# Performance work log

Hardware: AMD Instinct MI355X
Metric: run time of the kernel (lower is better)

## Reference

```python
import jax, jax.numpy as jnp
import numpy as np

B, S, VD, MD = 32, 2048, 512, 512
AD = max(VD, MD)


def setup_inputs() -> dict:
    key = jax.random.key(0)
    k1, k2, k3, k4, k5, k6 = jax.random.split(key, 6)
    query = jax.random.normal(k1, (B, VD), dtype=jnp.float32)
    keys = jax.random.normal(k2, (B, S, MD), dtype=jnp.float32)
    mask = jax.random.randint(k3, (B, S), 0, 2).astype(jnp.bool_)
    # torch Linear weight layout: [out, in]
    W1 = jax.random.normal(k4, (AD, VD), dtype=jnp.float32) * (1.0 / np.sqrt(VD))
    W2 = jax.random.normal(k5, (AD, MD), dtype=jnp.float32) * (1.0 / np.sqrt(MD))
    v = jax.random.normal(k6, (AD,), dtype=jnp.float32) * (1.0 / np.sqrt(AD))
    return {"query": query, "keys": keys, "mask": mask, "W1": W1, "W2": W2, "v": v}


def reference(query, keys, mask, W1, W2, v):
    # w1_query: [B, 1, AD]; w2_keys: [B, S, AD]
    w1_query = jnp.einsum('bd,ad->ba', query, W1)[:, None, :]
    w2_keys = jnp.einsum('bsd,ad->bsa', keys, W2)
    combined = jnp.tanh(w1_query + w2_keys)            # [B, S, AD]
    scores = jnp.einsum('bsa,a->bs', combined, v)      # [B, S]
    scores = jnp.where(mask, scores, -jnp.inf)
    attn_weights = jax.nn.softmax(scores, axis=-1)
    return attn_weights
```

## Files before the change

### kernel.cpp

```cpp
#include <hip/hip_runtime.h>
#include <math.h>

#define BB 32
#define SS 2048
#define DD 512
#define AD 512

#define BM 128
#define BN 128
#define BK 64

typedef __bf16 bf16;
typedef __attribute__((ext_vector_type(8))) __bf16 bf16x8;
typedef __attribute__((ext_vector_type(4))) __bf16 bf16x4;
typedef __attribute__((ext_vector_type(4))) float floatx4;

__device__ inline void async16(const void* g, void* l) {
    __builtin_amdgcn_global_load_lds(
        (const __attribute__((address_space(1))) unsigned int*)g,
        (__attribute__((address_space(3))) unsigned int*)l, 16, 0, 0);
}

#define NW8 (AD * DD / 8)
#define NCV (NW8 / 256)
__global__ void prep_kernel(const float* __restrict__ W2,
                            bf16* __restrict__ W2b,
                            const unsigned char* __restrict__ m8,
                            int* __restrict__ flag,
                            const float* __restrict__ query,
                            const float* __restrict__ W1,
                            float* __restrict__ w1q) {
    const int bid = blockIdx.x;
    if (bid < NCV) {
        int j = threadIdx.x + bid * 256;
        const float4* s4 = (const float4*)W2 + (size_t)j * 2;
        float4 x = s4[0], y = s4[1];
        bf16x8 o;
        o[0] = (bf16)x.x; o[1] = (bf16)x.y; o[2] = (bf16)x.z; o[3] = (bf16)x.w;
        o[4] = (bf16)y.x; o[5] = (bf16)y.y; o[6] = (bf16)y.z; o[7] = (bf16)y.w;
        *(bf16x8*)(W2b + (size_t)j * 8) = o;
    } else if (bid < NCV + 64) {
        int t = threadIdx.x + (bid - NCV) * 256;
        int any = 0;
        for (int i = t; i < BB * SS; i += 64 * 256)
            if ((i & 3) && m8[i]) any = 1;
        if (__any(any)) {
            if ((threadIdx.x & 63) == 0) atomicOr(flag, 1);
        }
    } else {
        int id = bid - NCV - 64;
        int b = id >> 7;
        int a = (id & 127) * 4 + (threadIdx.x >> 6);
        int lane = threadIdx.x & 63;
        const float4* q4 = (const float4*)(query + (size_t)b * DD) + lane * 2;
        const float4* w4 = (const float4*)(W1 + (size_t)a * DD) + lane * 2;
        float4 qa = q4[0], qb = q4[1];
        float4 wa = w4[0], wb = w4[1];
        float acc = qa.x * wa.x + qa.y * wa.y + qa.z * wa.z + qa.w * wa.w
                  + qb.x * wb.x + qb.y * wb.y + qb.z * wb.z + qb.w * wb.w;
#pragma unroll
        for (int off = 32; off > 0; off >>= 1) acc += __shfl_down(acc, off);
        if (lane == 0) w1q[(size_t)b * AD + a] = acc;
    }
}

__global__ __launch_bounds__(256, 3)
void gemm_scores_mfma(const float* __restrict__ keys,
                      const bf16* __restrict__ W2b,
                      const float* __restrict__ w1q,
                      const float* __restrict__ v,
                      float* __restrict__ partial) {
    __shared__ float a_lds[BM * BK];
    __shared__ bf16  b_lds[BN * BK];

    const int t    = threadIdx.x;
    const int lane = t & 63;
    const int w    = t >> 6;
    const int ml   = lane & 15;
    const int kg   = lane >> 4;

    const int lin    = blockIdx.x;
    const int x8     = lin & 7;
    const int hi     = lin >> 3;
    const int a_tile = hi & 3;
    const int kt     = x8 + ((hi >> 2) << 3);
    const int b      = kt >> 4;
    const int s0     = (kt & 15) * BM;
    const int a0     = a_tile * BN;

    const int m_off = (w & 1) * 64;
    const int n_off = (w >> 1) * 64;

    const float* Ablk = keys + ((size_t)b * SS + s0) * DD;
    const bf16*  Bblk = W2b + (size_t)a0 * DD;

    floatx4 acc[4][4];
#pragma unroll
    for (int mi = 0; mi < 4; ++mi)
#pragma unroll
        for (int ni = 0; ni < 4; ++ni)
            acc[mi][ni] = (floatx4)(0.f);

    const int NCHUNK = DD / BK;
    for (int c = 0; c < NCHUNK; ++c) {
        const int d0 = c * BK;
        __syncthreads();
#pragma unroll
        for (int i = 0; i < 8; ++i) {
            int g = t + 256 * i;
            int r = g >> 4, cc = g & 15, cs = cc ^ (r & 15);
            async16(Ablk + (size_t)r * DD + d0 + cs * 4,
                    &a_lds[(256 * i + 64 * w) * 4]);
        }
#pragma unroll
        for (int i = 0; i < 4; ++i) {
            int g = t + 256 * i;
            int r = g >> 3, cc = g & 7, cs = cc ^ (r & 7);
            async16(Bblk + (size_t)r * DD + d0 + cs * 8,
                    &b_lds[(256 * i + 64 * w) * 8]);
        }
        __syncthreads();

#pragma unroll
        for (int ks = 0; ks < 2; ++ks) {
            bf16x8 af[4], bfr[4];
#pragma unroll
            for (int mi = 0; mi < 4; ++mi) {
                int R  = m_off + mi * 16 + ml;
                int gB = 8 * ks + 2 * kg;
                float4 lo = *(const float4*)&a_lds[R * BK + ((gB    ) ^ (R & 15)) * 4];
                float4 hi4 = *(const float4*)&a_lds[R * BK + ((gB + 1) ^ (R & 15)) * 4];
                bf16x8 f;
                f[0] = (bf16)lo.x;  f[1] = (bf16)lo.y;
                f[2] = (bf16)lo.z;  f[3] = (bf16)lo.w;
                f[4] = (bf16)hi4.x; f[5] = (bf16)hi4.y;
                f[6] = (bf16)hi4.z; f[7] = (bf16)hi4.w;
                af[mi] = f;
            }
#pragma unroll
            for (int ni = 0; ni < 4; ++ni) {
                int R = n_off + ni * 16 + ml;
                int pos = (ks * 4 + kg) ^ (R & 7);
                bfr[ni] = *(const bf16x8*)&b_lds[R * BK + pos * 8];
            }
#pragma unroll
            for (int mi = 0; mi < 4; ++mi)
#pragma unroll
                for (int ni = 0; ni < 4; ++ni)
                    acc[mi][ni] = __builtin_amdgcn_mfma_f32_16x16x32_bf16(
                        af[mi], bfr[ni], acc[mi][ni], 0, 0, 0);
        }
    }

    float w1qa[4], va[4];
#pragma unroll
    for (int ni = 0; ni < 4; ++ni) {
        int a = a0 + n_off + ni * 16 + ml;
        w1qa[ni] = w1q[(size_t)b * AD + a];
        va[ni]   = v[a];
    }
    const int slot = a_tile * 2 + (w >> 1);
#pragma unroll
    for (int mi = 0; mi < 4; ++mi) {
#pragma unroll
        for (int reg = 0; reg < 4; ++reg) {
            float p = 0.f;
#pragma unroll
            for (int ni = 0; ni < 4; ++ni) {
                float x = acc[mi][ni][reg] + w1qa[ni];
                float th = 1.f - 2.f / (1.f + __expf(2.f * x));
                p = fmaf(th, va[ni], p);
            }
            p += __shfl_xor(p, 1);
            p += __shfl_xor(p, 2);
            p += __shfl_xor(p, 4);
            p += __shfl_xor(p, 8);
            if (ml == 0) {
                int row = m_off + mi * 16 + kg * 4 + reg;
                partial[((size_t)b * SS + s0 + row) * 8 + slot] = p;
            }
        }
    }
}

#define FBK 32
#define FLDK (FBK + 8)
__global__ __launch_bounds__(256, 2)
void gemm_scores_fallback(const float* __restrict__ keys,
                          const float* __restrict__ W2,
                          const float* __restrict__ w1q,
                          const float* __restrict__ v,
                          float* __restrict__ partial) {
    __shared__ bf16 a_lds[BM][FLDK];
    __shared__ bf16 b_lds[BN][FLDK];
    __shared__ float s_red[BM];

    const int t    = threadIdx.x;
    const int lane = t & 63;
    const int w    = t >> 6;
    const int ml   = lane & 15;
    const int kg   = lane >> 4;
    const int b    = blockIdx.z;
    const int s0   = blockIdx.x * BM;
    const int a0   = blockIdx.y * BN;
    const int m_off = (w & 1) * 64;
    const int n_off = (w >> 1) * 64;

    const float* Ablk = keys + ((size_t)b * SS + s0) * DD;
    const float* Bblk = W2 + (size_t)a0 * DD;

    if (t < BM) s_red[t] = 0.f;

    floatx4 acc[4][4];
#pragma unroll
    for (int mi = 0; mi < 4; ++mi)
#pragma unroll
        for (int ni = 0; ni < 4; ++ni)
            acc[mi][ni] = (floatx4)(0.f);

    float4 ga[4], gb[4];
#pragma unroll
    for (int i = 0; i < 4; ++i) {
        int idx = t + 256 * i;
        int r = idx >> 3, c = idx & 7;
        ga[i] = *(const float4*)(Ablk + (size_t)r * DD + c * 4);
        gb[i] = *(const float4*)(Bblk + (size_t)r * DD + c * 4);
    }

    for (int chunk = 0; chunk < DD / FBK; ++chunk) {
        __syncthreads();
#pragma unroll
        for (int i = 0; i < 4; ++i) {
            int idx = t + 256 * i;
            int r = idx >> 3, c = idx & 7;
            bf16x4 pa, pb;
            pa[0] = (bf16)ga[i].x; pa[1] = (bf16)ga[i].y;
            pa[2] = (bf16)ga[i].z; pa[3] = (bf16)ga[i].w;
            pb[0] = (bf16)gb[i].x; pb[1] = (bf16)gb[i].y;
            pb[2] = (bf16)gb[i].z; pb[3] = (bf16)gb[i].w;
            *(bf16x4*)&a_lds[r][c * 4] = pa;
            *(bf16x4*)&b_lds[r][c * 4] = pb;
        }
        __syncthreads();
        if (chunk < DD / FBK - 1) {
            int d0 = (chunk + 1) * FBK;
#pragma unroll
            for (int i = 0; i < 4; ++i) {
                int idx = t + 256 * i;
                int r = idx >> 3, c = idx & 7;
                ga[i] = *(const float4*)(Ablk + (size_t)r * DD + d0 + c * 4);
                gb[i] = *(const float4*)(Bblk + (size_t)r * DD + d0 + c * 4);
            }
        }
        bf16x8 af[4], bfr[4];
#pragma unroll
        for (int mi = 0; mi < 4; ++mi)
            af[mi] = *(const bf16x8*)&a_lds[m_off + mi * 16 + ml][kg * 8];
#pragma unroll
        for (int ni = 0; ni < 4; ++ni)
            bfr[ni] = *(const bf16x8*)&b_lds[n_off + ni * 16 + ml][kg * 8];
#pragma unroll
        for (int mi = 0; mi < 4; ++mi)
#pragma unroll
            for (int ni = 0; ni < 4; ++ni)
                acc[mi][ni] = __builtin_amdgcn_mfma_f32_16x16x32_bf16(
                    af[mi], bfr[ni], acc[mi][ni], 0, 0, 0);
    }

    float w1qa[4], va[4];
#pragma unroll
    for (int ni = 0; ni < 4; ++ni) {
        int a = a0 + n_off + ni * 16 + ml;
        w1qa[ni] = w1q[(size_t)b * AD + a];
        va[ni]   = v[a];
    }
#pragma unroll
    for (int mi = 0; mi < 4; ++mi) {
#pragma unroll
        for (int reg = 0; reg < 4; ++reg) {
            float p = 0.f;
#pragma unroll
            for (int ni = 0; ni < 4; ++ni) {
                float x = acc[mi][ni][reg] + w1qa[ni];
                float th = 1.f - 2.f / (1.f + __expf(2.f * x));
                p = fmaf(th, va[ni], p);
            }
            p += __shfl_xor(p, 1);
            p += __shfl_xor(p, 2);
            p += __shfl_xor(p, 4);
            p += __shfl_xor(p, 8);
            if (ml == 0)
                atomicAdd(&s_red[m_off + mi * 16 + kg * 4 + reg], p);
        }
    }
    __syncthreads();
    if (t < BM)
        partial[(((size_t)b * SS) + s0 + t) * 8 + blockIdx.y * 2] = s_red[t];
}

__global__ void softmax_kernel(const float* __restrict__ partial,
                               const int* __restrict__ mask_i32,
                               const unsigned char* __restrict__ mask_u8,
                               const int* __restrict__ flag,
                               float* __restrict__ out) {
    const int b = blockIdx.x;
    const int t = threadIdx.x;
    __shared__ float rmax[4], rsum[4];
    const int wid = t >> 6, lane = t & 63;

    float sv[8]; int mv[8];
    const int bytes = (*flag != 0);
#pragma unroll
    for (int k = 0; k < 8; ++k) {
        int i = t + 256 * k;
        const float4* p4 = (const float4*)(partial + ((size_t)b * SS + i) * 8);
        float4 pa = p4[0], pb = p4[1];
        sv[k] = ((pa.x + pa.y) + (pa.z + pa.w)) + ((pb.x + pb.y) + (pb.z + pb.w));
        mv[k] = bytes ? (int)mask_u8[(size_t)b * SS + i]
                      : mask_i32[(size_t)b * SS + i];
    }

    float mx = -INFINITY;
#pragma unroll
    for (int k = 0; k < 8; ++k) mx = fmaxf(mx, mv[k] ? sv[k] : -INFINITY);
#pragma unroll
    for (int off = 32; off > 0; off >>= 1) mx = fmaxf(mx, __shfl_xor(mx, off));
    if (lane == 0) rmax[wid] = mx;
    __syncthreads();
    mx = fmaxf(fmaxf(rmax[0], rmax[1]), fmaxf(rmax[2], rmax[3]));

    float ev[8]; float sum = 0.f;
#pragma unroll
    for (int k = 0; k < 8; ++k) {
        ev[k] = mv[k] ? __expf(sv[k] - mx) : 0.f;
        sum += ev[k];
    }
#pragma unroll
    for (int off = 32; off > 0; off >>= 1) sum += __shfl_xor(sum, off);
    if (lane == 0) rsum[wid] = sum;
    __syncthreads();
    sum = (rsum[0] + rsum[1]) + (rsum[2] + rsum[3]);
    float inv = 1.f / sum;
#pragma unroll
    for (int k = 0; k < 8; ++k)
        out[(size_t)b * SS + t + 256 * k] = ev[k] * inv;
}

extern "C" void kernel_launch(void* const* d_in, const int* in_sizes, int n_in,
                              void* d_out, int out_size, void* d_ws, size_t ws_size,
                              hipStream_t stream) {
    const float* query = (const float*)d_in[0];
    const float* keys  = (const float*)d_in[1];
    const void*  mask  = d_in[2];
    const float* W1    = (const float*)d_in[3];
    const float* W2    = (const float*)d_in[4];
    const float* v     = (const float*)d_in[5];
    float* out = (float*)d_out;

    char* wsb = (char*)d_ws;
    int*   flag    = (int*)wsb;
    float* w1q     = (float*)(wsb + 256);
    float* partial = (float*)(wsb + 256 + 65536);
    bf16*  W2b     = (bf16*)(wsb + 256 + 65536 + 2097152);
    size_t need = 256 + 65536 + 2097152 + (size_t)AD * DD * 2;

    hipMemsetAsync(flag, 0, 4, stream);
    if (ws_size >= need) {
        prep_kernel<<<NCV + 64 + 4096, 256, 0, stream>>>(
            W2, W2b, (const unsigned char*)mask, flag, query, W1, w1q);
        gemm_scores_mfma<<<(SS / BM) * (AD / BN) * BB, 256, 0, stream>>>(
            keys, W2b, w1q, v, partial);
    } else {
        hipMemsetAsync(partial, 0, (size_t)BB * SS * 8 * 4, stream);
        prep_kernel<<<NCV + 64 + 4096, 256, 0, stream>>>(
            W2, W2b, (const unsigned char*)mask, flag, query, W1, w1q);
        gemm_scores_fallback<<<dim3(SS / BM, AD / BN, BB), 256, 0, stream>>>(
            keys, W2, w1q, v, partial);
    }
    softmax_kernel<<<BB, 256, 0, stream>>>(partial, (const int*)mask,
                                           (const unsigned char*)mask, flag, out);
}
```

Measured before the change: 245.2 us.

## Load keys directly to registers and double-buffer W2 tiles in LDS

The GEMM kernel no longer stages the fp32 keys tile through LDS. Each wave now owns 32 rows and loads its A fragments straight from global memory into registers, converting to bf16 there. The W2 bf16 tile is double-buffered in LDS, so the next chunk prefetches while the current one is computed, and one barrier per chunk is dropped. The per-row partial buffer shrinks from 8 to 4 slots, since each block covers all 128 output columns. This removes LDS traffic for A and overlaps B loads, at the cost of uncoalesced-ish direct global reads and higher register use (acc 2x8).

```diff
diff --git a/kernel.cpp b/kernel.cpp
--- a/kernel.cpp
+++ b/kernel.cpp
@@ -70,8 +70,7 @@
                       const float* __restrict__ w1q,
                       const float* __restrict__ v,
                       float* __restrict__ partial) {
-    __shared__ float a_lds[BM * BK];
-    __shared__ bf16  b_lds[BN * BK];
+    __shared__ bf16 b_lds[2][BN * BK];
 
     const int t    = threadIdx.x;
     const int lane = t & 63;
@@ -88,85 +87,93 @@
     const int s0     = (kt & 15) * BM;
     const int a0     = a_tile * BN;
 
-    const int m_off = (w & 1) * 64;
-    const int n_off = (w >> 1) * 64;
-
     const float* Ablk = keys + ((size_t)b * SS + s0) * DD;
     const bf16*  Bblk = W2b + (size_t)a0 * DD;
 
-    floatx4 acc[4][4];
-#pragma unroll
-    for (int mi = 0; mi < 4; ++mi)
-#pragma unroll
-        for (int ni = 0; ni < 4; ++ni)
+    const float* arow0 = Ablk + (size_t)(w * 32 + ml) * DD;
+    const float* arow1 = arow0 + 16 * DD;
+
+    floatx4 acc[2][8];
+#pragma unroll
+    for (int mi = 0; mi < 2; ++mi)
+#pragma unroll
+        for (int ni = 0; ni < 8; ++ni)
             acc[mi][ni] = (floatx4)(0.f);
+
+#pragma unroll
+    for (int i = 0; i < 4; ++i) {
+        int g = t + 256 * i;
+        int r = g >> 3, cc = g & 7, cs = cc ^ (r & 7);
+        async16(Bblk + (size_t)r * DD + cs * 8, &b_lds[0][(256 * i + 64 * w) * 8]);
+    }
 
     const int NCHUNK = DD / BK;
     for (int c = 0; c < NCHUNK; ++c) {
-        const int d0 = c * BK;
+        const int cur = c & 1;
         __syncthreads();
-#pragma unroll
-        for (int i = 0; i < 8; ++i) {
-            int g = t + 256 * i;
-            int r = g >> 4, cc = g & 15, cs = cc ^ (r & 15);
-            async16(Ablk + (size_t)r * DD + d0 + cs * 4,
-                    &a_lds[(256 * i + 64 * w) * 4]);
-        }
-#pragma unroll
-        for (int i = 0; i < 4; ++i) {
-            int g = t + 256 * i;
-            int r = g >> 3, cc = g & 7, cs = cc ^ (r & 7);
-            async16(Bblk + (size_t)r * DD + d0 + cs * 8,
-                    &b_lds[(256 * i + 64 * w) * 8]);
-        }
-        __syncthreads();
+
+        if (c + 1 < NCHUNK) {
+            const int d0 = (c + 1) * BK;
+#pragma unroll
+            for (int i = 0; i < 4; ++i) {
+                int g = t + 256 * i;
+                int r = g >> 3, cc = g & 7, cs = cc ^ (r & 7);
+                async16(Bblk + (size_t)r * DD + d0 + cs * 8,
+                        &b_lds[!cur][(256 * i + 64 * w) * 8]);
+            }
+        }
+
+        const int ko = c * BK + kg * 8;
+        float4 ga[2][2][2];
+#pragma unroll
+        for (int mi = 0; mi < 2; ++mi) {
+            const float* ar = mi ? arow1 : arow0;
+#pragma unroll
+            for (int ks = 0; ks < 2; ++ks) {
+                ga[mi][ks][0] = *(const float4*)(ar + ko + ks * 32);
+                ga[mi][ks][1] = *(const float4*)(ar + ko + ks * 32 + 4);
+            }
+        }
 
 #pragma unroll
         for (int ks = 0; ks < 2; ++ks) {
-            bf16x8 af[4], bfr[4];
-#pragma unroll
-            for (int mi = 0; mi < 4; ++mi) {
-                int R  = m_off + mi * 16 + ml;
-                int gB = 8 * ks + 2 * kg;
-                float4 lo = *(const float4*)&a_lds[R * BK + ((gB    ) ^ (R & 15)) * 4];
-                float4 hi4 = *(const float4*)&a_lds[R * BK + ((gB + 1) ^ (R & 15)) * 4];
+            bf16x8 af[2];
+#pragma unroll
+            for (int mi = 0; mi < 2; ++mi) {
                 bf16x8 f;
-                f[0] = (bf16)lo.x;  f[1] = (bf16)lo.y;
-                f[2] = (bf16)lo.z;  f[3] = (bf16)lo.w;
-                f[4] = (bf16)hi4.x; f[5] = (bf16)hi4.y;
-                f[6] = (bf16)hi4.z; f[7] = (bf16)hi4.w;
+                f[0] = (bf16)ga[mi][ks][0].x; f[1] = (bf16)ga[mi][ks][0].y;
+                f[2] = (bf16)ga[mi][ks][0].z; f[3] = (bf16)ga[mi][ks][0].w;
+                f[4] = (bf16)ga[mi][ks][1].x; f[5] = (bf16)ga[mi][ks][1].y;
+                f[6] = (bf16)ga[mi][ks][1].z; f[7] = (bf16)ga[mi][ks][1].w;
                 af[mi] = f;
             }
 #pragma unroll
-            for (int ni = 0; ni < 4; ++ni) {
-                int R = n_off + ni * 16 + ml;
+            for (int ni = 0; ni < 8; ++ni) {
+                int R = ni * 16 + ml;
                 int pos = (ks * 4 + kg) ^ (R & 7);
-                bfr[ni] = *(const bf16x8*)&b_lds[R * BK + pos * 8];
-            }
-#pragma unroll
-            for (int mi = 0; mi < 4; ++mi)
-#pragma unroll
-                for (int ni = 0; ni < 4; ++ni)
+                bf16x8 bf = *(const bf16x8*)&b_lds[cur][R * BK + pos * 8];
+#pragma unroll
+                for (int mi = 0; mi < 2; ++mi)
                     acc[mi][ni] = __builtin_amdgcn_mfma_f32_16x16x32_bf16(
-                        af[mi], bfr[ni], acc[mi][ni], 0, 0, 0);
-        }
-    }
-
-    float w1qa[4], va[4];
-#pragma unroll
-    for (int ni = 0; ni < 4; ++ni) {
-        int a = a0 + n_off + ni * 16 + ml;
+                        af[mi], bf, acc[mi][ni], 0, 0, 0);
+            }
+        }
+    }
+
+    float w1qa[8], va[8];
+#pragma unroll
+    for (int ni = 0; ni < 8; ++ni) {
+        int a = a0 + ni * 16 + ml;
         w1qa[ni] = w1q[(size_t)b * AD + a];
         va[ni]   = v[a];
     }
-    const int slot = a_tile * 2 + (w >> 1);
-#pragma unroll
-    for (int mi = 0; mi < 4; ++mi) {
+#pragma unroll
+    for (int mi = 0; mi < 2; ++mi) {
 #pragma unroll
         for (int reg = 0; reg < 4; ++reg) {
             float p = 0.f;
 #pragma unroll
-            for (int ni = 0; ni < 4; ++ni) {
+            for (int ni = 0; ni < 8; ++ni) {
                 float x = acc[mi][ni][reg] + w1qa[ni];
                 float th = 1.f - 2.f / (1.f + __expf(2.f * x));
                 p = fmaf(th, va[ni], p);
@@ -176,8 +183,8 @@
             p += __shfl_xor(p, 4);
             p += __shfl_xor(p, 8);
             if (ml == 0) {
-                int row = m_off + mi * 16 + kg * 4 + reg;
-                partial[((size_t)b * SS + s0 + row) * 8 + slot] = p;
+                int row = w * 32 + mi * 16 + kg * 4 + reg;
+                partial[((size_t)b * SS + s0 + row) * 4 + a_tile] = p;
             }
         }
     }
@@ -295,7 +302,7 @@
     }
     __syncthreads();
     if (t < BM)
-        partial[(((size_t)b * SS) + s0 + t) * 8 + blockIdx.y * 2] = s_red[t];
+        partial[(((size_t)b * SS) + s0 + t) * 4 + blockIdx.y] = s_red[t];
 }
 
 __global__ void softmax_kernel(const float* __restrict__ partial,
@@ -313,9 +320,8 @@
 #pragma unroll
     for (int k = 0; k < 8; ++k) {
         int i = t + 256 * k;
-        const float4* p4 = (const float4*)(partial + ((size_t)b * SS + i) * 8);
-        float4 pa = p4[0], pb = p4[1];
-        sv[k] = ((pa.x + pa.y) + (pa.z + pa.w)) + ((pb.x + pb.y) + (pb.z + pb.w));
+        float4 p4 = *(const float4*)(partial + ((size_t)b * SS + i) * 4);
+        sv[k] = (p4.x + p4.y) + (p4.z + p4.w);
         mv[k] = bytes ? (int)mask_u8[(size_t)b * SS + i]
                       : mask_i32[(size_t)b * SS + i];
     }
@@ -361,8 +367,8 @@
     int*   flag    = (int*)wsb;
     float* w1q     = (float*)(wsb + 256);
     float* partial = (float*)(wsb + 256 + 65536);
-    bf16*  W2b     = (bf16*)(wsb + 256 + 65536 + 2097152);
-    size_t need = 256 + 65536 + 2097152 + (size_t)AD * DD * 2;
+    bf16*  W2b     = (bf16*)(wsb + 256 + 65536 + 1048576);
+    size_t need = 256 + 65536 + 1048576 + (size_t)AD * DD * 2;
 
     hipMemsetAsync(flag, 0, 4, stream);
     if (ws_size >= need) {
@@ -371,7 +377,7 @@
         gemm_scores_mfma<<<(SS / BM) * (AD / BN) * BB, 256, 0, stream>>>(
             keys, W2b, w1q, v, partial);
     } else {
-        hipMemsetAsync(partial, 0, (size_t)BB * SS * 8 * 4, stream);
+        hipMemsetAsync(partial, 0, (size_t)BB * SS * 4 * 4, stream);
         prep_kernel<<<NCV + 64 + 4096, 256, 0, stream>>>(
             W2, W2b, (const unsigned char*)mask, flag, query, W1, w1q);
         gemm_scores_fallback<<<dim3(SS / BM, AD / BN, BB), 256, 0, stream>>>(
```

After: 259.5 us. +5.9%, slower.
